# Kernel optimization log

Hardware: AMD Instinct MI355X
Metric: run time of the kernel (lower is better)

The kernel has to match this reference:

```python
import jax, jax.numpy as jnp
import numpy as np

B, N, NIN, NH, NOUT = 32, 64, 256, 256, 2
E = N * (N - 1)
BN_EPS = 1e-5


def _xavier(k, fan_in, fan_out):
    return jax.random.normal(k, (fan_in, fan_out), jnp.float32) * np.sqrt(2.0 / (fan_in + fan_out))


def _mlp_params(key, n_in, n_hid, n_out):
    k1, k2 = jax.random.split(key)
    return {
        'w1': _xavier(k1, n_in, n_hid), 'b1': jnp.full((n_hid,), 0.1, jnp.float32),
        'w2': _xavier(k2, n_hid, n_out), 'b2': jnp.full((n_out,), 0.1, jnp.float32),
        'g': jnp.ones((n_out,), jnp.float32), 'beta': jnp.zeros((n_out,), jnp.float32),
    }


def setup_inputs() -> dict:
    key = jax.random.key(0)
    ks = jax.random.split(key, 7)
    inputs = jax.random.normal(ks[0], (B, N, NIN), jnp.float32)
    # fully-connected directed graph w/o self loops: edge e = (send i, recv j), i != j
    idx = np.array([(i, j) for i in range(N) for j in range(N) if i != j], dtype=np.int64)
    rel_send = np.zeros((E, N), np.float32)
    rel_rec = np.zeros((E, N), np.float32)
    rel_send[np.arange(E), idx[:, 0]] = 1.0
    rel_rec[np.arange(E), idx[:, 1]] = 1.0
    out = {'inputs': inputs, 'rel_rec': jnp.asarray(rel_rec), 'rel_send': jnp.asarray(rel_send)}
    for name, (ni, nh, no), k in [('mlp1', (NIN, NH, NH), ks[1]),
                                  ('mlp2', (2 * NH, NH, NH), ks[2]),
                                  ('mlp3', (NH, NH, NH), ks[3]),
                                  ('mlp4', (3 * NH, NH, NH), ks[4])]:
        p = _mlp_params(k, ni, nh, no)
        for pk, pv in p.items():
            out[f'{name}_{pk}'] = pv
    out['fc_w'] = _xavier(ks[5], NH, NOUT)
    out['fc_b'] = jnp.full((NOUT,), 0.1, jnp.float32)
    return out


def _mlp(x, w1, b1, w2, b2, g, beta):
    # Linear -> ELU -> Linear -> ELU -> BatchNorm1d (training-mode batch stats, biased var)
    h = jax.nn.elu(x @ w1 + b1)
    h = jax.nn.elu(h @ w2 + b2)
    mean = h.mean(axis=(0, 1))
    var = h.var(axis=(0, 1))
    return (h - mean) * jax.lax.rsqrt(var + BN_EPS) * g + beta


def reference(inputs, rel_rec, rel_send,
              mlp1_w1, mlp1_b1, mlp1_w2, mlp1_b2, mlp1_g, mlp1_beta,
              mlp2_w1, mlp2_b1, mlp2_w2, mlp2_b2, mlp2_g, mlp2_beta,
              mlp3_w1, mlp3_b1, mlp3_w2, mlp3_b2, mlp3_g, mlp3_beta,
              mlp4_w1, mlp4_b1, mlp4_w2, mlp4_b2, mlp4_g, mlp4_beta,
              fc_w, fc_b):
    x = _mlp(inputs, mlp1_w1, mlp1_b1, mlp1_w2, mlp1_b2, mlp1_g, mlp1_beta)  # [B,N,NH]
    # node2edge: gather sender/receiver node features per edge
    s = jnp.einsum('en,bnh->beh', rel_send, x)
    r = jnp.einsum('en,bnh->beh', rel_rec, x)
    x = jnp.concatenate([s, r], axis=-1)  # [B,E,2*NH]
    x = _mlp(x, mlp2_w1, mlp2_b1, mlp2_w2, mlp2_b2, mlp2_g, mlp2_beta)
    x_skip = x
    # edge2node: scatter-sum incoming edges per node, normalized by N
    inc = jnp.einsum('en,beh->bnh', rel_rec, x) / N
    x = _mlp(inc, mlp3_w1, mlp3_b1, mlp3_w2, mlp3_b2, mlp3_g, mlp3_beta)
    s = jnp.einsum('en,bnh->beh', rel_send, x)
    r = jnp.einsum('en,bnh->beh', rel_rec, x)
    x = jnp.concatenate([s, r, x_skip], axis=-1)  # [B,E,3*NH]
    x = _mlp(x, mlp4_w1, mlp4_b1, mlp4_w2, mlp4_b2, mlp4_g, mlp4_beta)
    return x @ fc_w + fc_b  # [B,E,NOUT]
```

## Files before the change

kernel.cpp:

```cpp
#include <hip/hip_runtime.h>

typedef __bf16 bf16_t;
typedef __bf16 bf16x8 __attribute__((ext_vector_type(8)));
typedef float  f32x4  __attribute__((ext_vector_type(4)));

#define NB    64
#define EB    4032
#define BATCH 32
#define H     256
#define M_EDGE (BATCH*EB)
#define M_NODE (BATCH*NB)
#define BN_EPS 1e-5f

__device__ __forceinline__ void load_lds16(const void* g, void* l) {
    __builtin_amdgcn_global_load_lds(
        (const __attribute__((address_space(1))) unsigned int*)g,
        (__attribute__((address_space(3))) unsigned int*)l, 16, 0, 0);
}
__device__ __forceinline__ float elu(float v) { return v > 0.f ? v : __expf(v) - 1.f; }

template<bool AF32>
__global__ __launch_bounds__(256, 3)
void fused_mlp(const void* __restrict__ A0v,
               const bf16_t* __restrict__ W1f, const float* __restrict__ b1,
               const bf16_t* __restrict__ W2f, const float* __restrict__ b2,
               bf16_t* __restrict__ out, float* __restrict__ stats)
{
    const int m0 = blockIdx.x * 64;
    const int tid = threadIdx.x, wave = tid >> 6, lane = tid & 63;
    const int l15 = lane & 15, quad = lane >> 4;
    const int row = tid >> 2;
    const int c0 = (tid & 3) * 64;

    __shared__ bf16_t h1s[64 * 264];
    __shared__ float  sred[512];

    sred[tid] = 0.f; sred[256 + tid] = 0.f;

    if (AF32) {
        const float* af = (const float*)A0v + (size_t)(m0 + row) * 256 + c0;
#pragma unroll
        for (int j = 0; j < 8; ++j) {
            float4 lo = *(const float4*)(af + j * 8);
            float4 hi = *(const float4*)(af + j * 8 + 4);
            bf16x8 v;
            v[0]=(bf16_t)lo.x; v[1]=(bf16_t)lo.y; v[2]=(bf16_t)lo.z; v[3]=(bf16_t)lo.w;
            v[4]=(bf16_t)hi.x; v[5]=(bf16_t)hi.y; v[6]=(bf16_t)hi.z; v[7]=(bf16_t)hi.w;
            *(bf16x8*)&h1s[row * 264 + c0 + j * 8] = v;
        }
    } else {
        const bf16_t* src = (const bf16_t*)A0v + (size_t)(m0 + row) * 256 + c0;
#pragma unroll
        for (int j = 0; j < 8; ++j)
            *(bf16x8*)&h1s[row * 264 + c0 + j * 8] = *(const bf16x8*)(src + j * 8);
    }

    const bf16_t* W1W = W1f + (size_t)wave * 16384;
    const bf16_t* W2W = W2f + (size_t)wave * 16384;

    bf16x8 bcur[4], bnxt[4];
#pragma unroll
    for (int u = 0; u < 4; ++u)
        bcur[u] = *(const bf16x8*)(W1W + u * 512 + lane * 8);
    __syncthreads();

    f32x4 acc[4][4];
#pragma unroll
    for (int a = 0; a < 4; ++a)
#pragma unroll
        for (int u = 0; u < 4; ++u) acc[a][u] = (f32x4){0.f, 0.f, 0.f, 0.f};

#pragma unroll
    for (int ks = 0; ks < 8; ++ks) {
        if (ks < 7) {
#pragma unroll
            for (int u = 0; u < 4; ++u)
                bnxt[u] = *(const bf16x8*)(W1W + (ks + 1) * 2048 + u * 512 + lane * 8);
        }
        bf16x8 afr[4];
#pragma unroll
        for (int a = 0; a < 4; ++a)
            afr[a] = *(const bf16x8*)&h1s[(a * 16 + l15) * 264 + ks * 32 + quad * 8];
#pragma unroll
        for (int a = 0; a < 4; ++a)
#pragma unroll
            for (int u = 0; u < 4; ++u)
                acc[a][u] = __builtin_amdgcn_mfma_f32_16x16x32_bf16(afr[a], bcur[u], acc[a][u], 0, 0, 0);
#pragma unroll
        for (int u = 0; u < 4; ++u) bcur[u] = bnxt[u];
    }

#pragma unroll
    for (int u = 0; u < 4; ++u)
        bcur[u] = *(const bf16x8*)(W2W + u * 512 + lane * 8);
    __syncthreads();

#pragma unroll
    for (int u = 0; u < 4; ++u) {
        int   col = wave * 64 + u * 16 + l15;
        float bv  = b1[col];
#pragma unroll
        for (int a = 0; a < 4; ++a)
#pragma unroll
            for (int r = 0; r < 4; ++r)
                h1s[(a * 16 + quad * 4 + r) * 264 + col] = (bf16_t)elu(acc[a][u][r] + bv);
    }
    __syncthreads();

#pragma unroll
    for (int a = 0; a < 4; ++a)
#pragma unroll
        for (int u = 0; u < 4; ++u) acc[a][u] = (f32x4){0.f, 0.f, 0.f, 0.f};
#pragma unroll
    for (int ks = 0; ks < 8; ++ks) {
        if (ks < 7) {
#pragma unroll
            for (int u = 0; u < 4; ++u)
                bnxt[u] = *(const bf16x8*)(W2W + (ks + 1) * 2048 + u * 512 + lane * 8);
        }
        bf16x8 afr[4];
#pragma unroll
        for (int a = 0; a < 4; ++a)
            afr[a] = *(const bf16x8*)&h1s[(a * 16 + l15) * 264 + ks * 32 + quad * 8];
#pragma unroll
        for (int a = 0; a < 4; ++a)
#pragma unroll
            for (int u = 0; u < 4; ++u)
                acc[a][u] = __builtin_amdgcn_mfma_f32_16x16x32_bf16(afr[a], bcur[u], acc[a][u], 0, 0, 0);
#pragma unroll
        for (int u = 0; u < 4; ++u) bcur[u] = bnxt[u];
    }
    __syncthreads();

#pragma unroll
    for (int u = 0; u < 4; ++u) {
        int   col = wave * 64 + u * 16 + l15;
        float bv  = b2[col];
        float s = 0.f, q = 0.f;
#pragma unroll
        for (int a = 0; a < 4; ++a)
#pragma unroll
            for (int r = 0; r < 4; ++r) {
                float v = elu(acc[a][u][r] + bv);
                h1s[(a * 16 + quad * 4 + r) * 264 + col] = (bf16_t)v;
                s += v; q += v * v;
            }
        s += __shfl_xor(s, 16); s += __shfl_xor(s, 32);
        q += __shfl_xor(q, 16); q += __shfl_xor(q, 32);
        if (quad == 0) { atomicAdd(&sred[col], s); atomicAdd(&sred[256 + col], q); }
    }
    __syncthreads();

#pragma unroll
    for (int p = 0; p < 8; ++p) {
        int idx = p * 256 + tid;
        int r = idx >> 5, ch = idx & 31;
        *(uint4*)&out[(size_t)(m0 + r) * H + ch * 8] = *(const uint4*)&h1s[r * 264 + ch * 8];
    }
    atomicAdd(&stats[tid],     sred[tid]);
    atomicAdd(&stats[H + tid], sred[256 + tid]);
}

__global__ __launch_bounds__(256)
void node_gemm(const bf16_t* __restrict__ A, const float* __restrict__ statsIn,
               const float* __restrict__ g, const float* __restrict__ beta, float Mcnt,
               const bf16_t* __restrict__ Wt, const float* __restrict__ bias,
               float* __restrict__ out)
{
    const int m0 = blockIdx.x * 64;
    const int nb = blockIdx.y * 256;
    const int tid = threadIdx.x, wave = tid >> 6, lane = tid & 63;
    const int l15 = lane & 15, quad = lane >> 4;
    const int row = tid >> 2;
    const int cx8 = (((tid & 3) ^ ((tid >> 3) & 3))) * 8;
    const int sl8 = (tid & 3) * 8;
    const int xq8 = (quad ^ ((l15 >> 1) & 3)) * 8;
    __shared__ bf16_t As[64 * 32];
    __shared__ bf16_t Bs[256 * 32];
    __shared__ float  ss[512];

    {
        float mean = statsIn[tid] / Mcnt;
        float var  = statsIn[256 + tid] / Mcnt - mean * mean;
        float scl  = g[tid] * rsqrtf(var + BN_EPS);
        ss[tid]       = scl;
        ss[256 + tid] = beta[tid] - mean * scl;
    }
    __syncthreads();

    f32x4 acc[4][4];
#pragma unroll
    for (int t = 0; t < 4; ++t)
#pragma unroll
        for (int u = 0; u < 4; ++u) acc[t][u] = (f32x4){0.f, 0.f, 0.f, 0.f};

    for (int k0 = 0; k0 < 256; k0 += 32) {
        {
            int kc = k0 + cx8;
            bf16x8 v = *(const bf16x8*)(A + (size_t)(m0 + row) * 256 + kc);
            bf16x8 w;
#pragma unroll
            for (int j = 0; j < 8; ++j)
                w[j] = (bf16_t)((float)v[j] * ss[kc + j] + ss[256 + kc + j]);
            *(bf16x8*)&As[row * 32 + sl8] = w;
        }
#pragma unroll
        for (int p = 0; p < 4; ++p)
            load_lds16(Wt + (size_t)(nb + p * 64 + row) * 256 + k0 + cx8,
                       Bs + (p * 256 + wave * 64) * 8);
        __syncthreads();
        bf16x8 afr[4], bfr[4];
#pragma unroll
        for (int t = 0; t < 4; ++t)
            afr[t] = *(const bf16x8*)&As[(t * 16 + l15) * 32 + xq8];
#pragma unroll
        for (int u = 0; u < 4; ++u)
            bfr[u] = *(const bf16x8*)&Bs[(wave * 64 + u * 16 + l15) * 32 + xq8];
#pragma unroll
        for (int t = 0; t < 4; ++t)
#pragma unroll
            for (int u = 0; u < 4; ++u)
                acc[t][u] = __builtin_amdgcn_mfma_f32_16x16x32_bf16(afr[t], bfr[u], acc[t][u], 0, 0, 0);
        __syncthreads();
    }
#pragma unroll
    for (int u = 0; u < 4; ++u) {
        int col = nb + wave * 64 + u * 16 + l15;
        float bv = bias[col];
#pragma unroll
        for (int t = 0; t < 4; ++t)
#pragma unroll
            for (int r = 0; r < 4; ++r)
                out[(size_t)(m0 + t * 16 + quad * 4 + r) * 512 + col] = acc[t][u][r] + bv;
    }
}

__global__ __launch_bounds__(256, 3)
void m2_kernel(const float* __restrict__ PQ, const bf16_t* __restrict__ W2f,
               const float* __restrict__ b2, bf16_t* __restrict__ out,
               float* __restrict__ stats)
{
    const int m0 = blockIdx.x * 64;
    const int tid = threadIdx.x, wave = tid >> 6, lane = tid & 63;
    const int l15 = lane & 15, quad = lane >> 4;
    const int row = tid >> 2;
    const int c0 = (tid & 3) * 64;
    const int xq8 = (quad ^ ((l15 >> 1) & 3)) * 8;

    __shared__ bf16_t h1s[8 * 2048];
    __shared__ float  sred[512];

    sred[tid] = 0.f; sred[256 + tid] = 0.f;

    const int bb  = m0 / EB;
    const int e0  = m0 - bb * EB;
    const int sn0 = e0 / (NB - 1);
    const int rr0 = e0 - sn0 * (NB - 1);

    {
        int t  = rr0 + row;
        int wrap = (t >= NB - 1) ? 1 : 0;
        int sn = sn0 + wrap;
        int rr = t - (wrap ? (NB - 1) : 0);
        int rc = rr + (rr >= sn ? 1 : 0);
        const float* Prow = PQ + (size_t)(bb * NB + sn) * 512;
        const float* Qrow = PQ + (size_t)(bb * NB + rc) * 512 + 256;
        const int rs = ((row >> 1) & 3);
#pragma unroll
        for (int j = 0; j < 8; ++j) {
            int c = c0 + j * 8;
            float4 p0 = *(const float4*)(Prow + c);
            float4 p1 = *(const float4*)(Prow + c + 4);
            float4 q0 = *(const float4*)(Qrow + c);
            float4 q1 = *(const float4*)(Qrow + c + 4);
            bf16x8 v;
            v[0]=(bf16_t)elu(p0.x+q0.x); v[1]=(bf16_t)elu(p0.y+q0.y);
            v[2]=(bf16_t)elu(p0.z+q0.z); v[3]=(bf16_t)elu(p0.w+q0.w);
            v[4]=(bf16_t)elu(p1.x+q1.x); v[5]=(bf16_t)elu(p1.y+q1.y);
            v[6]=(bf16_t)elu(p1.z+q1.z); v[7]=(bf16_t)elu(p1.w+q1.w);
            *(bf16x8*)&h1s[(c >> 5) * 2048 + row * 32 + ((((c >> 3) & 3) ^ rs) * 8)] = v;
        }
    }

    const bf16_t* W2W = W2f + (size_t)wave * 16384;
    bf16x8 bcur[4], bnxt[4];
#pragma unroll
    for (int u = 0; u < 4; ++u)
        bcur[u] = *(const bf16x8*)(W2W + u * 512 + lane * 8);
    __syncthreads();

    f32x4 acc[4][4];
#pragma unroll
    for (int a = 0; a < 4; ++a)
#pragma unroll
        for (int u = 0; u < 4; ++u) acc[a][u] = (f32x4){0.f, 0.f, 0.f, 0.f};

#pragma unroll
    for (int ks = 0; ks < 8; ++ks) {
        if (ks < 7) {
#pragma unroll
            for (int u = 0; u < 4; ++u)
                bnxt[u] = *(const bf16x8*)(W2W + (ks + 1) * 2048 + u * 512 + lane * 8);
        }
        bf16x8 afr[4];
#pragma unroll
        for (int a = 0; a < 4; ++a)
            afr[a] = *(const bf16x8*)&h1s[ks * 2048 + (a * 16 + l15) * 32 + xq8];
#pragma unroll
        for (int a = 0; a < 4; ++a)
#pragma unroll
            for (int u = 0; u < 4; ++u)
                acc[a][u] = __builtin_amdgcn_mfma_f32_16x16x32_bf16(afr[a], bcur[u], acc[a][u], 0, 0, 0);
#pragma unroll
        for (int u = 0; u < 4; ++u) bcur[u] = bnxt[u];
    }
    __syncthreads();

#pragma unroll
    for (int u = 0; u < 4; ++u) {
        const int col = wave * 64 + u * 16 + l15;
        const float bv = b2[col];
        const int ks = wave * 2 + (u >> 1);
        const int qw = (u & 1) * 2 + (l15 >> 3);
        const int j  = l15 & 7;
        float s = 0.f, q = 0.f;
#pragma unroll
        for (int a = 0; a < 4; ++a)
#pragma unroll
            for (int r = 0; r < 4; ++r) {
                float v = elu(acc[a][u][r] + bv);
                int rw = a * 16 + quad * 4 + r;
                int qp = qw ^ ((rw >> 1) & 3);
                h1s[ks * 2048 + rw * 32 + qp * 8 + j] = (bf16_t)v;
                s += v; q += v * v;
            }
        s += __shfl_xor(s, 16); s += __shfl_xor(s, 32);
        q += __shfl_xor(q, 16); q += __shfl_xor(q, 32);
        if (quad == 0) { atomicAdd(&sred[col], s); atomicAdd(&sred[256 + col], q); }
    }
    __syncthreads();

#pragma unroll
    for (int p = 0; p < 8; ++p) {
        int idx = p * 256 + tid;
        int r = idx >> 5, ch = idx & 31;
        *(uint4*)&out[(size_t)(m0 + r) * H + ch * 8] =
            *(const uint4*)&h1s[(ch >> 2) * 2048 + r * 32 + (((ch & 3) ^ ((r >> 1) & 3)) * 8)];
    }
    atomicAdd(&stats[tid],     sred[tid]);
    atomicAdd(&stats[H + tid], sred[256 + tid]);
}

__global__ __launch_bounds__(256, 3)
void m4_kernel(const bf16_t* __restrict__ h2, const bf16_t* __restrict__ Wskf,
               const float* __restrict__ RS, const bf16_t* __restrict__ W4f,
               const float* __restrict__ b2, bf16_t* __restrict__ out,
               float* __restrict__ stats)
{
    const int m0 = blockIdx.x * 64;
    const int tid = threadIdx.x, wave = tid >> 6, lane = tid & 63;
    const int l15 = lane & 15, quad = lane >> 4;
    const int row = tid >> 2;
    const int cx8 = (((tid & 3) ^ ((tid >> 3) & 3))) * 8;
    const int xq8 = (quad ^ ((l15 >> 1) & 3)) * 8;

    __shared__ bf16_t h1s[8 * 2048];
    __shared__ float  sred[512];

    sred[tid] = 0.f; sred[256 + tid] = 0.f;

    const int bb  = m0 / EB;
    const int e0  = m0 - bb * EB;
    const int sn0 = e0 / (NB - 1);
    const int rr0 = e0 - sn0 * (NB - 1);
    const float* RSb = RS + (size_t)(bb * NB) * 512;

#pragma unroll
    for (int ks = 0; ks < 8; ++ks)
        load_lds16(h2 + (size_t)(m0 + row) * 256 + ks * 32 + cx8,
                   h1s + ks * 2048 + wave * 512);

    f32x4 acc[4][4];
#pragma unroll
    for (int a = 0; a < 4; ++a)
#pragma unroll
        for (int r = 0; r < 4; ++r) {
            int ro = a * 16 + quad * 4 + r;
            int t  = rr0 + ro;
            int wrap = (t >= NB - 1) ? 1 : 0;
            int sn = sn0 + wrap;
            int rr = t - (wrap ? (NB - 1) : 0);
            int rc = rr + (rr >= sn ? 1 : 0);
            const float* Srow = RSb + (size_t)sn * 512;
            const float* Rrow = RSb + (size_t)rc * 512 + 256;
#pragma unroll
            for (int u = 0; u < 4; ++u) {
                int co = wave * 64 + u * 16 + l15;
                acc[a][u][r] = Srow[co] + Rrow[co];
            }
        }

    const bf16_t* WskW = Wskf + (size_t)wave * 16384;
    const bf16_t* W4W  = W4f  + (size_t)wave * 16384;

    bf16x8 bcur[4], bnxt[4];
#pragma unroll
    for (int u = 0; u < 4; ++u)
        bcur[u] = *(const bf16x8*)(WskW + u * 512 + lane * 8);
    __syncthreads();

#pragma unroll
    for (int ks = 0; ks < 8; ++ks) {
        if (ks < 7) {
#pragma unroll
            for (int u = 0; u < 4; ++u)
                bnxt[u] = *(const bf16x8*)(WskW + (ks + 1) * 2048 + u * 512 + lane * 8);
        }
        bf16x8 afr[4];
#pragma unroll
        for (int a = 0; a < 4; ++a)
            afr[a] = *(const bf16x8*)&h1s[ks * 2048 + (a * 16 + l15) * 32 + xq8];
#pragma unroll
        for (int a = 0; a < 4; ++a)
#pragma unroll
            for (int u = 0; u < 4; ++u)
                acc[a][u] = __builtin_amdgcn_mfma_f32_16x16x32_bf16(afr[a], bcur[u], acc[a][u], 0, 0, 0);
#pragma unroll
        for (int u = 0; u < 4; ++u) bcur[u] = bnxt[u];
    }

#pragma unroll
    for (int u = 0; u < 4; ++u)
        bcur[u] = *(const bf16x8*)(W4W + u * 512 + lane * 8);
    __syncthreads();

#pragma unroll
    for (int u = 0; u < 4; ++u) {
        const int ks = wave * 2 + (u >> 1);
        const int qw = (u & 1) * 2 + (l15 >> 3);
        const int j  = l15 & 7;
#pragma unroll
        for (int a = 0; a < 4; ++a)
#pragma unroll
            for (int r = 0; r < 4; ++r) {
                int rw = a * 16 + quad * 4 + r;
                int qp = qw ^ ((rw >> 1) & 3);
                h1s[ks * 2048 + rw * 32 + qp * 8 + j] = (bf16_t)elu(acc[a][u][r]);
            }
    }
    __syncthreads();

#pragma unroll
    for (int a = 0; a < 4; ++a)
#pragma unroll
        for (int u = 0; u < 4; ++u) acc[a][u] = (f32x4){0.f, 0.f, 0.f, 0.f};
#pragma unroll
    for (int ks = 0; ks < 8; ++ks) {
        if (ks < 7) {
#pragma unroll
            for (int u = 0; u < 4; ++u)
                bnxt[u] = *(const bf16x8*)(W4W + (ks + 1) * 2048 + u * 512 + lane * 8);
        }
        bf16x8 afr[4];
#pragma unroll
        for (int a = 0; a < 4; ++a)
            afr[a] = *(const bf16x8*)&h1s[ks * 2048 + (a * 16 + l15) * 32 + xq8];
#pragma unroll
        for (int a = 0; a < 4; ++a)
#pragma unroll
            for (int u = 0; u < 4; ++u)
                acc[a][u] = __builtin_amdgcn_mfma_f32_16x16x32_bf16(afr[a], bcur[u], acc[a][u], 0, 0, 0);
#pragma unroll
        for (int u = 0; u < 4; ++u) bcur[u] = bnxt[u];
    }
    __syncthreads();

#pragma unroll
    for (int u = 0; u < 4; ++u) {
        const int col = wave * 64 + u * 16 + l15;
        const float bv = b2[col];
        const int ks = wave * 2 + (u >> 1);
        const int qw = (u & 1) * 2 + (l15 >> 3);
        const int j  = l15 & 7;
        float s = 0.f, q = 0.f;
#pragma unroll
        for (int a = 0; a < 4; ++a)
#pragma unroll
            for (int r = 0; r < 4; ++r) {
                float v = elu(acc[a][u][r] + bv);
                int rw = a * 16 + quad * 4 + r;
                int qp = qw ^ ((rw >> 1) & 3);
                h1s[ks * 2048 + rw * 32 + qp * 8 + j] = (bf16_t)v;
                s += v; q += v * v;
            }
        s += __shfl_xor(s, 16); s += __shfl_xor(s, 32);
        q += __shfl_xor(q, 16); q += __shfl_xor(q, 32);
        if (quad == 0) { atomicAdd(&sred[col], s); atomicAdd(&sred[256 + col], q); }
    }
    __syncthreads();

#pragma unroll
    for (int p = 0; p < 8; ++p) {
        int idx = p * 256 + tid;
        int r = idx >> 5, ch = idx & 31;
        *(uint4*)&out[(size_t)(m0 + r) * H + ch * 8] =
            *(const uint4*)&h1s[(ch >> 2) * 2048 + r * 32 + (((ch & 3) ^ ((r >> 1) & 3)) * 8)];
    }
    atomicAdd(&stats[tid],     sred[tid]);
    atomicAdd(&stats[H + tid], sred[256 + tid]);
}

__global__ void prep(const float* __restrict__ w1a, bf16_t* __restrict__ wt1a,
                     const float* __restrict__ w1b, bf16_t* __restrict__ wt1b,
                     const float* __restrict__ w2b, bf16_t* __restrict__ wt2b,
                     const float* __restrict__ w3a, bf16_t* __restrict__ wt3a,
                     const float* __restrict__ w3b, bf16_t* __restrict__ wt3b,
                     const float* __restrict__ w4b, bf16_t* __restrict__ wt4b,
                     const float* __restrict__ w2a, bf16_t* __restrict__ wtpq,
                     const float* __restrict__ w4a, bf16_t* __restrict__ wtrs,
                     const float* __restrict__ b2a, float* __restrict__ biasPQ,
                     float* __restrict__ stats)
{
    int blk = blockIdx.x, tid = threadIdx.x;
    if (blk < 1536) {
        int grp = blk >> 8, lb = blk & 255;
        int idx = lb * 256 + tid;
        int k = idx >> 8, n = idx & 255;
        const float* w; bf16_t* wt;
        switch (grp) {
            case 0: w = w1a; wt = wt1a; break;
            case 1: w = w1b; wt = wt1b; break;
            case 2: w = w2b; wt = wt2b; break;
            case 3: w = w3a; wt = wt3a; break;
            case 4: w = w3b; wt = wt3b; break;
            default: w = w4b; wt = wt4b; break;
        }
        int wv = n >> 6, u = (n >> 4) & 3, l15 = n & 15;
        int ks = k >> 5, qd = (k >> 3) & 3, j = k & 7;
        wt[wv * 16384 + ks * 2048 + u * 512 + (qd * 16 + l15) * 8 + j] = (bf16_t)w[idx];
    } else if (blk < 2560) {
        int lb = blk - 1536;
        const float* w = (lb < 512) ? w2a : w4a;
        bf16_t* wt = (lb < 512) ? wtpq : wtrs;
        int c = lb & 511, k = tid;
        float v = (c < 256) ? w[k * 256 + c] : w[(256 + k) * 256 + (c - 256)];
        wt[c * 256 + k] = (bf16_t)v;
    } else if (blk == 2560) {
        biasPQ[tid] = b2a[tid];
        biasPQ[256 + tid] = 0.f;
    } else {
        for (int j = 0; j < 8; ++j) stats[j * 256 + tid] = 0.f;
    }
}

__global__ void prep2(const float* __restrict__ w4a, const float* __restrict__ stats2,
                      const float* __restrict__ g2, const float* __restrict__ be2,
                      const float* __restrict__ b4a, bf16_t* __restrict__ wt,
                      float* __restrict__ bias)
{
    __shared__ float sh2s[256];
    int blk = blockIdx.x, tid = threadIdx.x;
    float mean = stats2[tid] / (float)M_EDGE;
    float var  = stats2[256 + tid] / (float)M_EDGE - mean * mean;
    float scl  = g2[tid] * rsqrtf(var + BN_EPS);
    if (blk < 256) {
        int n = blk, k = tid;
        int wv = n >> 6, u = (n >> 4) & 3, l15 = n & 15;
        int ks = k >> 5, qd = (k >> 3) & 3, j = k & 7;
        wt[wv * 16384 + ks * 2048 + u * 512 + (qd * 16 + l15) * 8 + j] =
            (bf16_t)(w4a[(512 + tid) * 256 + blk] * scl);
    } else {
        sh2s[tid] = be2[tid] - mean * scl;
        __syncthreads();
        float acc = 0.f;
        for (int k = 0; k < 256; ++k)
            acc += sh2s[k] * w4a[(512 + k) * 256 + tid];
        bias[tid] = b4a[tid] + acc;
        bias[256 + tid] = 0.f;
    }
}

__global__ void edge2node(const bf16_t* __restrict__ x2, const float* __restrict__ stats2,
                          const float* __restrict__ g2, const float* __restrict__ be2,
                          bf16_t* __restrict__ inc)
{
    int bn = blockIdx.x, bb = bn >> 6, n = bn & 63;
    int g = threadIdx.x >> 5, t = threadIdx.x & 31;
    __shared__ float part[8][256];
    __shared__ float ss[512];
    {
        int c = threadIdx.x;
        float mean = stats2[c] / (float)M_EDGE;
        float var  = stats2[256 + c] / (float)M_EDGE - mean * mean;
        float scl  = g2[c] * rsqrtf(var + BN_EPS);
        ss[c]       = scl;
        ss[256 + c] = be2[c] - mean * scl;
    }
    const bf16_t* base = x2 + (size_t)bb * EB * H;
    float a[8] = {0.f,0.f,0.f,0.f,0.f,0.f,0.f,0.f};
    for (int i = g; i < NB; i += 8) {
        if (i == n) continue;
        int e = i * (NB - 1) + n - (n > i ? 1 : 0);
        bf16x8 v = *(const bf16x8*)&base[(size_t)e * H + t * 8];
#pragma unroll
        for (int j = 0; j < 8; ++j) a[j] += (float)v[j];
    }
#pragma unroll
    for (int j = 0; j < 8; ++j) part[g][t * 8 + j] = a[j];
    __syncthreads();
    int c = threadIdx.x;
    float s = 0.f;
#pragma unroll
    for (int g2i = 0; g2i < 8; ++g2i) s += part[g2i][c];
    inc[(size_t)bn * H + c] = (bf16_t)(s * (1.f / 64.f) * ss[c] + ss[256 + c] * (63.f / 64.f));
}

__global__ void fc_kernel(const bf16_t* __restrict__ x4, const float* __restrict__ stats4,
                          const float* __restrict__ g4, const float* __restrict__ be4,
                          const float* __restrict__ fcw, const float* __restrict__ fcb,
                          float* __restrict__ out)
{
    __shared__ float ss[512];
    {
        int c = threadIdx.x;
        float mean = stats4[c] / (float)M_EDGE;
        float var  = stats4[256 + c] / (float)M_EDGE - mean * mean;
        float scl  = g4[c] * rsqrtf(var + BN_EPS);
        ss[c]       = scl;
        ss[256 + c] = be4[c] - mean * scl;
    }
    __syncthreads();
    int row  = blockIdx.x * 8 + (threadIdx.x >> 5);
    int t    = threadIdx.x & 31;
    bf16x8 v8 = *(const bf16x8*)(x4 + (size_t)row * H + t * 8);
    float s0 = 0.f, s1 = 0.f;
#pragma unroll
    for (int j = 0; j < 8; ++j) {
        int c = t * 8 + j;
        float v = (float)v8[j] * ss[c] + ss[256 + c];
        s0 += v * fcw[c * 2];
        s1 += v * fcw[c * 2 + 1];
    }
#pragma unroll
    for (int off = 16; off; off >>= 1) {
        s0 += __shfl_down(s0, off, 32);
        s1 += __shfl_down(s1, off, 32);
    }
    if (t == 0) {
        out[(size_t)row * 2]     = s0 + fcb[0];
        out[(size_t)row * 2 + 1] = s1 + fcb[1];
    }
}

extern "C" void kernel_launch(void* const* d_in, const int* in_sizes, int n_in,
                              void* d_out, int out_size, void* d_ws, size_t ws_size,
                              hipStream_t stream)
{
    (void)in_sizes; (void)n_in; (void)out_size; (void)ws_size;
    const float* inp = (const float*)d_in[0];
    const float* w1a = (const float*)d_in[3];  const float* b1a = (const float*)d_in[4];
    const float* w1b = (const float*)d_in[5];  const float* b1b = (const float*)d_in[6];
    const float* g1  = (const float*)d_in[7];  const float* be1 = (const float*)d_in[8];
    const float* w2a = (const float*)d_in[9];  const float* b2a = (const float*)d_in[10];
    const float* w2b = (const float*)d_in[11]; const float* b2b = (const float*)d_in[12];
    const float* g2  = (const float*)d_in[13]; const float* be2 = (const float*)d_in[14];
    const float* w3a = (const float*)d_in[15]; const float* b3a = (const float*)d_in[16];
    const float* w3b = (const float*)d_in[17]; const float* b3b = (const float*)d_in[18];
    const float* g3  = (const float*)d_in[19]; const float* be3 = (const float*)d_in[20];
    const float* w4a = (const float*)d_in[21]; const float* b4a = (const float*)d_in[22];
    const float* w4b = (const float*)d_in[23]; const float* b4b = (const float*)d_in[24];
    const float* g4  = (const float*)d_in[25]; const float* be4 = (const float*)d_in[26];
    const float* fcw = (const float*)d_in[27]; const float* fcb = (const float*)d_in[28];

    char* p = (char*)d_ws;
    auto alloc = [&](size_t nbytes) { char* r = p; p += (nbytes + 255) & ~(size_t)255; return r; };

    bf16_t* wt1a = (bf16_t*)alloc(256 * 256 * 2);
    bf16_t* wt1b = (bf16_t*)alloc(256 * 256 * 2);
    bf16_t* wt2b = (bf16_t*)alloc(256 * 256 * 2);
    bf16_t* wt3a = (bf16_t*)alloc(256 * 256 * 2);
    bf16_t* wt3b = (bf16_t*)alloc(256 * 256 * 2);
    bf16_t* wt4b = (bf16_t*)alloc(256 * 256 * 2);
    bf16_t* wtpq = (bf16_t*)alloc(512 * 256 * 2);
    bf16_t* wtrs = (bf16_t*)alloc(512 * 256 * 2);
    bf16_t* wtsk = (bf16_t*)alloc(256 * 256 * 2);
    float*  biasPQ = (float*)alloc(512 * sizeof(float));
    float*  biasRS = (float*)alloc(512 * sizeof(float));
    float*  stats  = (float*)alloc(4 * 512 * sizeof(float));
    bf16_t* x1   = (bf16_t*)alloc((size_t)M_NODE * H * 2);
    bf16_t* incb = (bf16_t*)alloc((size_t)M_NODE * H * 2);
    bf16_t* x3   = (bf16_t*)alloc((size_t)M_NODE * H * 2);
    float*  PQ   = (float*)alloc((size_t)M_NODE * 512 * sizeof(float));
    float*  RS   = (float*)alloc((size_t)M_NODE * 512 * sizeof(float));
    bf16_t* h2   = (bf16_t*)alloc((size_t)M_EDGE * H * 2);
    bf16_t* h4   = (bf16_t*)alloc((size_t)M_EDGE * H * 2);

    prep<<<2562, 256, 0, stream>>>(w1a, wt1a, w1b, wt1b, w2b, wt2b, w3a, wt3a,
                                   w3b, wt3b, w4b, wt4b, w2a, wtpq, w4a, wtrs,
                                   b2a, biasPQ, stats);

    fused_mlp<true ><<<M_NODE / 64, 256, 0, stream>>>(inp, wt1a, b1a, wt1b, b1b, x1, stats + 0);

    { dim3 g(M_NODE / 64, 2);
      node_gemm<<<g, 256, 0, stream>>>(x1, stats + 0, g1, be1, (float)M_NODE, wtpq, biasPQ, PQ); }

    m2_kernel<<<M_EDGE / 64, 256, 0, stream>>>(PQ, wt2b, b2b, h2, stats + 512);

    edge2node<<<M_NODE, 256, 0, stream>>>(h2, stats + 512, g2, be2, incb);
    fused_mlp<false><<<M_NODE / 64, 256, 0, stream>>>(incb, wt3a, b3a, wt3b, b3b, x3, stats + 1024);

    prep2<<<257, 256, 0, stream>>>(w4a, stats + 512, g2, be2, b4a, wtsk, biasRS);
    { dim3 g(M_NODE / 64, 2);
      node_gemm<<<g, 256, 0, stream>>>(x3, stats + 1024, g3, be3, (float)M_NODE, wtrs, biasRS, RS); }

    m4_kernel<<<M_EDGE / 64, 256, 0, stream>>>(h2, wtsk, RS, wt4b, b4b, h4, stats + 1536);

    fc_kernel<<<M_EDGE / 8, 256, 0, stream>>>(h4, stats + 1536, g4, be4, fcw, fcb, (float*)d_out);
}
```

Measured before the change: 352.8 us.

## Halve node-kernel row tiles and stream fragment-packed weights in node_gemm

The node-level fused MLP and node GEMM kernels now process 32 rows per block instead of 64, doubling the grid so the small node problem (2048 rows) fills more compute units. node_gemm also drops its per-k-step LDS staging of the weight matrix and instead loads MFMA-fragment-packed weights straight from global into registers with double buffering, as fused_mlp already does. The A tile is fully normalized into swizzled LDS once up front. Weight traffic per block stays the same while rows per block halve, so total weight reads double.

Result: faster. 340.0 us (-3.6%).

```diff
diff --git a/kernel.cpp b/kernel.cpp
--- a/kernel.cpp
+++ b/kernel.cpp
@@ -26,13 +26,13 @@
                const bf16_t* __restrict__ W2f, const float* __restrict__ b2,
                bf16_t* __restrict__ out, float* __restrict__ stats)
 {
-    const int m0 = blockIdx.x * 64;
+    const int m0 = blockIdx.x * 32;
     const int tid = threadIdx.x, wave = tid >> 6, lane = tid & 63;
     const int l15 = lane & 15, quad = lane >> 4;
-    const int row = tid >> 2;
-    const int c0 = (tid & 3) * 64;
-
-    __shared__ bf16_t h1s[64 * 264];
+    const int row = tid >> 3;
+    const int c0 = (tid & 7) * 32;
+
+    __shared__ bf16_t h1s[32 * 264];
     __shared__ float  sred[512];
 
     sred[tid] = 0.f; sred[256 + tid] = 0.f;
@@ -40,7 +40,7 @@
     if (AF32) {
         const float* af = (const float*)A0v + (size_t)(m0 + row) * 256 + c0;
 #pragma unroll
-        for (int j = 0; j < 8; ++j) {
+        for (int j = 0; j < 4; ++j) {
             float4 lo = *(const float4*)(af + j * 8);
             float4 hi = *(const float4*)(af + j * 8 + 4);
             bf16x8 v;
@@ -51,7 +51,7 @@
     } else {
         const bf16_t* src = (const bf16_t*)A0v + (size_t)(m0 + row) * 256 + c0;
 #pragma unroll
-        for (int j = 0; j < 8; ++j)
+        for (int j = 0; j < 4; ++j)
             *(bf16x8*)&h1s[row * 264 + c0 + j * 8] = *(const bf16x8*)(src + j * 8);
     }
 
@@ -64,9 +64,9 @@
         bcur[u] = *(const bf16x8*)(W1W + u * 512 + lane * 8);
     __syncthreads();
 
-    f32x4 acc[4][4];
-#pragma unroll
-    for (int a = 0; a < 4; ++a)
+    f32x4 acc[2][4];
+#pragma unroll
+    for (int a = 0; a < 2; ++a)
 #pragma unroll
         for (int u = 0; u < 4; ++u) acc[a][u] = (f32x4){0.f, 0.f, 0.f, 0.f};
 
@@ -77,12 +77,12 @@
             for (int u = 0; u < 4; ++u)
                 bnxt[u] = *(const bf16x8*)(W1W + (ks + 1) * 2048 + u * 512 + lane * 8);
         }
-        bf16x8 afr[4];
-#pragma unroll
-        for (int a = 0; a < 4; ++a)
+        bf16x8 afr[2];
+#pragma unroll
+        for (int a = 0; a < 2; ++a)
             afr[a] = *(const bf16x8*)&h1s[(a * 16 + l15) * 264 + ks * 32 + quad * 8];
 #pragma unroll
-        for (int a = 0; a < 4; ++a)
+        for (int a = 0; a < 2; ++a)
 #pragma unroll
             for (int u = 0; u < 4; ++u)
                 acc[a][u] = __builtin_amdgcn_mfma_f32_16x16x32_bf16(afr[a], bcur[u], acc[a][u], 0, 0, 0);
@@ -100,7 +100,7 @@
         int   col = wave * 64 + u * 16 + l15;
         float bv  = b1[col];
 #pragma unroll
-        for (int a = 0; a < 4; ++a)
+        for (int a = 0; a < 2; ++a)
 #pragma unroll
             for (int r = 0; r < 4; ++r)
                 h1s[(a * 16 + quad * 4 + r) * 264 + col] = (bf16_t)elu(acc[a][u][r] + bv);
@@ -108,7 +108,7 @@
     __syncthreads();
 
 #pragma unroll
-    for (int a = 0; a < 4; ++a)
+    for (int a = 0; a < 2; ++a)
 #pragma unroll
         for (int u = 0; u < 4; ++u) acc[a][u] = (f32x4){0.f, 0.f, 0.f, 0.f};
 #pragma unroll
@@ -118,12 +118,12 @@
             for (int u = 0; u < 4; ++u)
                 bnxt[u] = *(const bf16x8*)(W2W + (ks + 1) * 2048 + u * 512 + lane * 8);
         }
-        bf16x8 afr[4];
-#pragma unroll
-        for (int a = 0; a < 4; ++a)
+        bf16x8 afr[2];
+#pragma unroll
+        for (int a = 0; a < 2; ++a)
             afr[a] = *(const bf16x8*)&h1s[(a * 16 + l15) * 264 + ks * 32 + quad * 8];
 #pragma unroll
-        for (int a = 0; a < 4; ++a)
+        for (int a = 0; a < 2; ++a)
 #pragma unroll
             for (int u = 0; u < 4; ++u)
                 acc[a][u] = __builtin_amdgcn_mfma_f32_16x16x32_bf16(afr[a], bcur[u], acc[a][u], 0, 0, 0);
@@ -138,7 +138,7 @@
         float bv  = b2[col];
         float s = 0.f, q = 0.f;
 #pragma unroll
-        for (int a = 0; a < 4; ++a)
+        for (int a = 0; a < 2; ++a)
 #pragma unroll
             for (int r = 0; r < 4; ++r) {
                 float v = elu(acc[a][u][r] + bv);
@@ -152,7 +152,7 @@
     __syncthreads();
 
 #pragma unroll
-    for (int p = 0; p < 8; ++p) {
+    for (int p = 0; p < 4; ++p) {
         int idx = p * 256 + tid;
         int r = idx >> 5, ch = idx & 31;
         *(uint4*)&out[(size_t)(m0 + r) * H + ch * 8] = *(const uint4*)&h1s[r * 264 + ch * 8];
@@ -161,22 +161,21 @@
     atomicAdd(&stats[H + tid], sred[256 + tid]);
 }
 
-__global__ __launch_bounds__(256)
+__global__ __launch_bounds__(256, 3)
 void node_gemm(const bf16_t* __restrict__ A, const float* __restrict__ statsIn,
                const float* __restrict__ g, const float* __restrict__ beta, float Mcnt,
-               const bf16_t* __restrict__ Wt, const float* __restrict__ bias,
+               const bf16_t* __restrict__ Wf, const float* __restrict__ bias,
                float* __restrict__ out)
 {
-    const int m0 = blockIdx.x * 64;
+    const int m0 = blockIdx.x * 32;
     const int nb = blockIdx.y * 256;
     const int tid = threadIdx.x, wave = tid >> 6, lane = tid & 63;
     const int l15 = lane & 15, quad = lane >> 4;
-    const int row = tid >> 2;
-    const int cx8 = (((tid & 3) ^ ((tid >> 3) & 3))) * 8;
-    const int sl8 = (tid & 3) * 8;
+    const int row = tid >> 3;
+    const int c0 = (tid & 7) * 32;
     const int xq8 = (quad ^ ((l15 >> 1) & 3)) * 8;
-    __shared__ bf16_t As[64 * 32];
-    __shared__ bf16_t Bs[256 * 32];
+
+    __shared__ bf16_t As[8 * 1024];
     __shared__ float  ss[512];
 
     {
@@ -188,50 +187,63 @@
     }
     __syncthreads();
 
-    f32x4 acc[4][4];
-#pragma unroll
-    for (int t = 0; t < 4; ++t)
-#pragma unroll
-        for (int u = 0; u < 4; ++u) acc[t][u] = (f32x4){0.f, 0.f, 0.f, 0.f};
-
-    for (int k0 = 0; k0 < 256; k0 += 32) {
-        {
-            int kc = k0 + cx8;
-            bf16x8 v = *(const bf16x8*)(A + (size_t)(m0 + row) * 256 + kc);
+    {
+        const bf16_t* Ar = A + (size_t)(m0 + row) * 256 + c0;
+        const int rs = (row >> 1) & 3;
+#pragma unroll
+        for (int j = 0; j < 4; ++j) {
+            int c = c0 + j * 8;
+            bf16x8 v = *(const bf16x8*)(Ar + j * 8);
             bf16x8 w;
 #pragma unroll
-            for (int j = 0; j < 8; ++j)
-                w[j] = (bf16_t)((float)v[j] * ss[kc + j] + ss[256 + kc + j]);
-            *(bf16x8*)&As[row * 32 + sl8] = w;
-        }
-#pragma unroll
-        for (int p = 0; p < 4; ++p)
-            load_lds16(Wt + (size_t)(nb + p * 64 + row) * 256 + k0 + cx8,
-                       Bs + (p * 256 + wave * 64) * 8);
-        __syncthreads();
-        bf16x8 afr[4], bfr[4];
-#pragma unroll
-        for (int t = 0; t < 4; ++t)
-            afr[t] = *(const bf16x8*)&As[(t * 16 + l15) * 32 + xq8];
-#pragma unroll
-        for (int u = 0; u < 4; ++u)
-            bfr[u] = *(const bf16x8*)&Bs[(wave * 64 + u * 16 + l15) * 32 + xq8];
-#pragma unroll
-        for (int t = 0; t < 4; ++t)
-#pragma unroll
-            for (int u = 0; u < 4; ++u)
-                acc[t][u] = __builtin_amdgcn_mfma_f32_16x16x32_bf16(afr[t], bfr[u], acc[t][u], 0, 0, 0);
-        __syncthreads();
-    }
+            for (int e = 0; e < 8; ++e)
+                w[e] = (bf16_t)((float)v[e] * ss[c + e] + ss[256 + c + e]);
+            *(bf16x8*)&As[(c >> 5) * 1024 + row * 32 + ((((c >> 3) & 3) ^ rs) * 8)] = w;
+        }
+    }
+
+    const bf16_t* WW = Wf + (size_t)blockIdx.y * 65536 + (size_t)wave * 16384;
+    bf16x8 bcur[4], bnxt[4];
+#pragma unroll
+    for (int u = 0; u < 4; ++u)
+        bcur[u] = *(const bf16x8*)(WW + u * 512 + lane * 8);
+    __syncthreads();
+
+    f32x4 acc[2][4];
+#pragma unroll
+    for (int a = 0; a < 2; ++a)
+#pragma unroll
+        for (int u = 0; u < 4; ++u) acc[a][u] = (f32x4){0.f, 0.f, 0.f, 0.f};
+
+#pragma unroll
+    for (int ks = 0; ks < 8; ++ks) {
+        if (ks < 7) {
+#pragma unroll
+            for (int u = 0; u < 4; ++u)
+                bnxt[u] = *(const bf16x8*)(WW + (ks + 1) * 2048 + u * 512 + lane * 8);
+        }
+        bf16x8 afr[2];
+#pragma unroll
+        for (int a = 0; a < 2; ++a)
+            afr[a] = *(const bf16x8*)&As[ks * 1024 + (a * 16 + l15) * 32 + xq8];
+#pragma unroll
+        for (int a = 0; a < 2; ++a)
+#pragma unroll
+            for (int u = 0; u < 4; ++u)
+                acc[a][u] = __builtin_amdgcn_mfma_f32_16x16x32_bf16(afr[a], bcur[u], acc[a][u], 0, 0, 0);
+#pragma unroll
+        for (int u = 0; u < 4; ++u) bcur[u] = bnxt[u];
+    }
+
 #pragma unroll
     for (int u = 0; u < 4; ++u) {
         int col = nb + wave * 64 + u * 16 + l15;
         float bv = bias[col];
 #pragma unroll
-        for (int t = 0; t < 4; ++t)
+        for (int a = 0; a < 2; ++a)
 #pragma unroll
             for (int r = 0; r < 4; ++r)
-                out[(size_t)(m0 + t * 16 + quad * 4 + r) * 512 + col] = acc[t][u][r] + bv;
+                out[(size_t)(m0 + a * 16 + quad * 4 + r) * 512 + col] = acc[a][u][r] + bv;
     }
 }
 
@@ -544,7 +556,10 @@
         bf16_t* wt = (lb < 512) ? wtpq : wtrs;
         int c = lb & 511, k = tid;
         float v = (c < 256) ? w[k * 256 + c] : w[(256 + k) * 256 + (c - 256)];
-        wt[c * 256 + k] = (bf16_t)v;
+        int half = c >> 8, n = c & 255;
+        int wv = n >> 6, u = (n >> 4) & 3, l15 = n & 15;
+        int ks = k >> 5, qd = (k >> 3) & 3, j = k & 7;
+        wt[half * 65536 + wv * 16384 + ks * 2048 + u * 512 + (qd * 16 + l15) * 8 + j] = (bf16_t)v;
     } else if (blk == 2560) {
         biasPQ[tid] = b2a[tid];
         biasPQ[256 + tid] = 0.f;
@@ -699,18 +714,18 @@
                                    w3b, wt3b, w4b, wt4b, w2a, wtpq, w4a, wtrs,
                                    b2a, biasPQ, stats);
 
-    fused_mlp<true ><<<M_NODE / 64, 256, 0, stream>>>(inp, wt1a, b1a, wt1b, b1b, x1, stats + 0);
-
-    { dim3 g(M_NODE / 64, 2);
+    fused_mlp<true ><<<M_NODE / 32, 256, 0, stream>>>(inp, wt1a, b1a, wt1b, b1b, x1, stats + 0);
+
+    { dim3 g(M_NODE / 32, 2);
       node_gemm<<<g, 256, 0, stream>>>(x1, stats + 0, g1, be1, (float)M_NODE, wtpq, biasPQ, PQ); }
 
     m2_kernel<<<M_EDGE / 64, 256, 0, stream>>>(PQ, wt2b, b2b, h2, stats + 512);
 
     edge2node<<<M_NODE, 256, 0, stream>>>(h2, stats + 512, g2, be2, incb);
-    fused_mlp<false><<<M_NODE / 64, 256, 0, stream>>>(incb, wt3a, b3a, wt3b, b3b, x3, stats + 1024);
+    fused_mlp<false><<<M_NODE / 32, 256, 0, stream>>>(incb, wt3a, b3a, wt3b, b3b, x3, stats + 1024);
 
     prep2<<<257, 256, 0, stream>>>(w4a, stats + 512, g2, be2, b4a, wtsk, biasRS);
-    { dim3 g(M_NODE / 64, 2);
+    { dim3 g(M_NODE / 32, 2);
       node_gemm<<<g, 256, 0, stream>>>(x3, stats + 1024, g3, be3, (float)M_NODE, wtrs, biasRS, RS); }
 
     m4_kernel<<<M_EDGE / 64, 256, 0, stream>>>(h2, wtsk, RS, wt4b, b4b, h4, stats + 1536);
```
